# Optimization experiments

Measured on AMD Instinct MI355X. Metric: run time of the kernel, lower is better.

The kernel has to match this reference:

```python
import jax, jax.numpy as jnp
import numpy as np


def setup_inputs() -> dict:
    key = jax.random.key(0)
    k = jax.random.split(key, 5)
    C, Cb = 128, 64
    x = jax.random.normal(k[0], (8, C, 64, 64), dtype=jnp.float32)
    s_in = 1.0 / np.sqrt(C)
    s_b = 1.0 / np.sqrt(Cb)
    w_theta = jax.random.normal(k[1], (Cb, C), dtype=jnp.float32) * s_in
    w_phi = jax.random.normal(k[2], (Cb, C), dtype=jnp.float32) * s_in
    w_g = jax.random.normal(k[3], (Cb, C), dtype=jnp.float32) * s_in
    w_last = jax.random.normal(k[4], (C, Cb), dtype=jnp.float32) * s_b
    return {"x": x, "w_theta": w_theta, "w_phi": w_phi, "w_g": w_g, "w_last": w_last}


def reference(x, w_theta, w_phi, w_g, w_last):
    B, C, H, W = x.shape
    xf = x.reshape(B, C, H * W)            # [B, C, N]
    theta = jnp.einsum('kc,bcn->bkn', w_theta, xf)   # [B, Cb, N]
    phi = jnp.einsum('kc,bcn->bkn', w_phi, xf)       # [B, Cb, N]
    g = jnp.einsum('kc,bcn->bkn', w_g, xf)           # [B, Cb, N]
    # attention over spatial positions: [B, N, N]
    attn = jax.nn.softmax(jnp.einsum('bkn,bkm->bnm', theta, phi), axis=-1)
    y = jnp.einsum('bnm,bkm->bkn', attn, g)          # [B, Cb, N]
    out = jnp.einsum('ck,bkn->bcn', w_last, y).reshape(B, C, H, W)
    return out + x
```

## Files before the change

### kernel.cpp

```cpp
#include <hip/hip_runtime.h>
#include <stdint.h>

typedef _Float16 h8v __attribute__((ext_vector_type(8)));
typedef _Float16 h4v __attribute__((ext_vector_type(4)));
typedef float f4v __attribute__((ext_vector_type(4)));
typedef _Float16 f16;

#define NB 8
#define CC 128
#define CB 64
#define NN 4096
#define L2E 1.4426950408889634f

__global__ __launch_bounds__(256) void pack_w(
    const float* __restrict__ wth, const float* __restrict__ wph,
    const float* __restrict__ wg,  const float* __restrict__ wl,
    f16* __restrict__ wthp, f16* __restrict__ wphp,
    f16* __restrict__ wgp,  f16* __restrict__ wlp)
{
    const int t = blockIdx.x * 256 + threadIdx.x;
    for (int i = t; i < 8192; i += 2048){
        const int j = i & 7, lane = (i >> 3) & 63, kc = (i >> 9) & 3, ks = i >> 11;
        const int row = ks * 16 + (lane & 15);
        const int col = kc * 32 + ((lane >> 4) & 3) * 8 + j;
        wthp[i] = (f16)(wth[row * CC + col] * L2E);
        wphp[i] = (f16)(wph[row * CC + col]);
        wgp [i] = (f16)(wg [row * CC + col]);
    }
    for (int i = t; i < 8192; i += 2048){
        const int j = i & 7, lane = (i >> 3) & 63, kc = (i >> 9) & 1, cs = i >> 10;
        const int row = cs * 16 + (lane & 15);
        const int col = kc * 32 + ((lane >> 4) & 3) * 8 + j;
        wlp[i] = (f16)(wl[row * CB + col]);
    }
}

__global__ __launch_bounds__(256) void proj_kernel(
    const float* __restrict__ x, const f16* __restrict__ wthp,
    const f16* __restrict__ wphp, const f16* __restrict__ wgp,
    f16* __restrict__ thetaT, f16* __restrict__ phiT, f16* __restrict__ gbuf)
{
    __shared__ __align__(16) f16 xT[64][136];
    __shared__ __align__(16) f16 rep[4][16 * 72];
    const int b  = blockIdx.x & 7;
    const int n0 = (blockIdx.x >> 3) << 6;
    const int t  = threadIdx.x;

    #pragma unroll
    for (int i = 0; i < 8; i++){
        int v  = t + 256 * i;
        int c  = v >> 4;
        int j0 = (v & 15) << 2;
        const f4v xv = *(const f4v*)&x[((size_t)(b * CC + c)) * NN + n0 + j0];
        #pragma unroll
        for (int jj = 0; jj < 4; jj++) xT[j0 + jj][c] = (f16)xv[jj];
    }
    __syncthreads();

    const int w = t >> 6, lane = t & 63, quad = lane >> 4, l15 = lane & 15;
    const int rrow = lane >> 3, rcol = (lane & 7) * 8;

    h8v bx[4];
    #pragma unroll
    for (int kc = 0; kc < 4; kc++)
        bx[kc] = *(const h8v*)&xT[w * 16 + l15][kc * 32 + quad * 8];

    #pragma unroll
    for (int m3 = 0; m3 < 2; m3++){
        const f16* WP = (m3 == 0) ? wthp : wphp;
        f16* OUT      = (m3 == 0) ? thetaT : phiT;
        for (int ks = 0; ks < 4; ks++){
            f4v acc = {0.f, 0.f, 0.f, 0.f};
            #pragma unroll
            for (int kc = 0; kc < 4; kc++){
                const h8v af = *(const h8v*)&WP[(ks * 4 + kc) * 512 + lane * 8];
                acc = __builtin_amdgcn_mfma_f32_16x16x32_f16(af, bx[kc], acc, 0, 0, 0);
            }
            h4v pv;
            #pragma unroll
            for (int r = 0; r < 4; r++) pv[r] = (f16)acc[r];
            *(h4v*)&rep[w][l15 * 72 + ks * 16 + quad * 4] = pv;
        }
        #pragma unroll
        for (int j = 0; j < 2; j++){
            const h8v vv = *(const h8v*)&rep[w][(rrow + 8 * j) * 72 + rcol];
            *(h8v*)&OUT[((size_t)(b * NN + n0 + w * 16 + rrow + 8 * j)) * CB + rcol] = vv;
        }
    }

    h8v bw[4];
    #pragma unroll
    for (int kc = 0; kc < 4; kc++)
        bw[kc] = *(const h8v*)&wgp[(w * 4 + kc) * 512 + lane * 8];
    for (int ns = 0; ns < 4; ns++){
        f4v acc = {0.f, 0.f, 0.f, 0.f};
        #pragma unroll
        for (int kc = 0; kc < 4; kc++){
            const h8v af = *(const h8v*)&xT[ns * 16 + l15][kc * 32 + quad * 8];
            acc = __builtin_amdgcn_mfma_f32_16x16x32_f16(af, bw[kc], acc, 0, 0, 0);
        }
        h4v pv;
        #pragma unroll
        for (int r = 0; r < 4; r++) pv[r] = (f16)acc[r];
        *(h4v*)&rep[w][l15 * 72 + ns * 16 + quad * 4] = pv;
    }
    #pragma unroll
    for (int j = 0; j < 2; j++){
        const h8v vv = *(const h8v*)&rep[w][(rrow + 8 * j) * 72 + rcol];
        *(h8v*)&gbuf[((size_t)(b * CB + w * 16 + rrow + 8 * j)) * NN + n0 + rcol] = vv;
    }
}

union StageOrOut {
    struct { f16 ph[2][64 * 72]; f16 g[2][64 * 72]; } s;
    float fO[128][68];
};

__global__ __launch_bounds__(256) void attn_kernel(
    const f16* __restrict__ thetaT, const f16* __restrict__ phiT,
    const f16* __restrict__ gbuf, const f16* __restrict__ wlp,
    const float* __restrict__ x, float* __restrict__ out)
{
    __shared__ __align__(16) StageOrOut sh;
    __shared__ __align__(16) f16 plds[4][16 * 72];

    const int b  = blockIdx.x & 7;
    const int q0 = (blockIdx.x >> 3) << 6;
    const int t  = threadIdx.x;
    const int w = t >> 6, lane = t & 63, quad = lane >> 4, l15 = lane & 15;
    const int n0 = q0 + w * 16;

    const size_t trow = ((size_t)(b * NN + n0 + l15)) * CB;
    const h8v a0 = *(const h8v*)&thetaT[trow + quad * 8];
    const h8v a1 = *(const h8v*)&thetaT[trow + 32 + quad * 8];

    const int r0 = t >> 3, r1 = r0 + 32, c = (t & 7) * 8;
    const f16* pphi0 = phiT + ((size_t)(b * NN + r0)) * CB + c;
    const f16* pphi1 = phiT + ((size_t)(b * NN + r1)) * CB + c;
    const f16* pg0   = gbuf + ((size_t)(b * CB + r0)) * NN + c;
    const f16* pg1   = gbuf + ((size_t)(b * CB + r1)) * NN + c;
    const int lA = r0 * 72 + c, lB = r1 * 72 + c;

    h8v nA = *(const h8v*)pphi0;
    h8v nB = *(const h8v*)pphi1;
    h8v nC = *(const h8v*)pg0;
    h8v nD = *(const h8v*)pg1;
    *(h8v*)&sh.s.ph[0][lA] = nA;  *(h8v*)&sh.s.ph[0][lB] = nB;
    *(h8v*)&sh.s.g [0][lA] = nC;  *(h8v*)&sh.s.g [0][lB] = nD;

    float mrun = -1e30f, lrun = 0.f;
    f4v o[4];
    const f4v zf = {0.f, 0.f, 0.f, 0.f};
    #pragma unroll
    for (int tt = 0; tt < 4; tt++) o[tt] = zf;

    f16* const pw = &plds[w][0];

    for (int kb = 0; kb < 64; kb++){
        const int pb = kb & 1;
        __syncthreads();
        if (kb < 63){
            pphi0 += (size_t)64 * CB;  pphi1 += (size_t)64 * CB;
            pg0 += 64;                 pg1 += 64;
            nA = *(const h8v*)pphi0;   nB = *(const h8v*)pphi1;
            nC = *(const h8v*)pg0;     nD = *(const h8v*)pg1;
        }

        f4v s[4];
        #pragma unroll
        for (int tt = 0; tt < 4; tt++){
            const f16* pr = &sh.s.ph[pb][(tt * 16 + l15) * 72];
            const h8v pb0 = *(const h8v*)(pr + quad * 8);
            const h8v pb1 = *(const h8v*)(pr + 32 + quad * 8);
            f4v sv = zf;
            sv = __builtin_amdgcn_mfma_f32_16x16x32_f16(pb0, a0, sv, 0, 0, 0);
            sv = __builtin_amdgcn_mfma_f32_16x16x32_f16(pb1, a1, sv, 0, 0, 0);
            s[tt] = sv;
        }
        float smax = fmaxf(fmaxf(s[0][0], s[0][1]), fmaxf(s[0][2], s[0][3]));
        #pragma unroll
        for (int tt = 1; tt < 4; tt++)
            smax = fmaxf(smax, fmaxf(fmaxf(s[tt][0], s[tt][1]), fmaxf(s[tt][2], s[tt][3])));
        smax = fmaxf(smax, __shfl_xor(smax, 16));
        smax = fmaxf(smax, __shfl_xor(smax, 32));
        const float mn = fmaxf(mrun, smax);
        const float alpha = __builtin_amdgcn_exp2f(mrun - mn);
        mrun = mn;
        float lsum = 0.f;
        #pragma unroll
        for (int tt = 0; tt < 4; tt++){
            h4v pv;
            #pragma unroll
            for (int r = 0; r < 4; r++){
                float p = __builtin_amdgcn_exp2f(s[tt][r] - mn);
                lsum += p;
                pv[r] = (f16)p;
            }
            *(h4v*)&pw[l15 * 72 + tt * 16 + quad * 4] = pv;
        }
        lrun = lrun * alpha + lsum;
        #pragma unroll
        for (int tt = 0; tt < 4; tt++)
            #pragma unroll
            for (int r = 0; r < 4; r++)
                o[tt][r] *= alpha;

        const h8v pa0 = *(const h8v*)&pw[l15 * 72 + quad * 8];
        const h8v pa1 = *(const h8v*)&pw[l15 * 72 + 32 + quad * 8];

        #pragma unroll
        for (int tt = 0; tt < 4; tt++){
            const f16* gr = &sh.s.g[pb][(tt * 16 + l15) * 72];
            const h8v gb0 = *(const h8v*)(gr + quad * 8);
            const h8v gb1 = *(const h8v*)(gr + 32 + quad * 8);
            o[tt] = __builtin_amdgcn_mfma_f32_16x16x32_f16(gb0, pa0, o[tt], 0, 0, 0);
            o[tt] = __builtin_amdgcn_mfma_f32_16x16x32_f16(gb1, pa1, o[tt], 0, 0, 0);
        }

        if (kb < 63){
            const int nb = pb ^ 1;
            *(h8v*)&sh.s.ph[nb][lA] = nA;  *(h8v*)&sh.s.ph[nb][lB] = nB;
            *(h8v*)&sh.s.g [nb][lA] = nC;  *(h8v*)&sh.s.g [nb][lB] = nD;
        }
    }

    lrun += __shfl_xor(lrun, 16);
    lrun += __shfl_xor(lrun, 32);
    const float inv = 1.0f / lrun;

    #pragma unroll
    for (int tt = 0; tt < 4; tt++){
        h4v yv;
        #pragma unroll
        for (int r = 0; r < 4; r++) yv[r] = (f16)(o[tt][r] * inv);
        *(h4v*)&pw[l15 * 72 + tt * 16 + quad * 4] = yv;
    }

    __syncthreads();

    const h8v yB0 = *(const h8v*)&pw[l15 * 72 + quad * 8];
    const h8v yB1 = *(const h8v*)&pw[l15 * 72 + 32 + quad * 8];
    #pragma unroll
    for (int cs = 0; cs < 8; cs++){
        const h8v wa0 = *(const h8v*)&wlp[(cs * 2 + 0) * 512 + lane * 8];
        const h8v wa1 = *(const h8v*)&wlp[(cs * 2 + 1) * 512 + lane * 8];
        f4v acc = zf;
        acc = __builtin_amdgcn_mfma_f32_16x16x32_f16(wa0, yB0, acc, 0, 0, 0);
        acc = __builtin_amdgcn_mfma_f32_16x16x32_f16(wa1, yB1, acc, 0, 0, 0);
        #pragma unroll
        for (int r = 0; r < 4; r++)
            sh.fO[cs * 16 + quad * 4 + r][w * 16 + l15] = acc[r];
    }
    __syncthreads();

    #pragma unroll
    for (int i = 0; i < 8; i++){
        const int row = i * 16 + (t >> 4);
        const int nf  = (t & 15) * 4;
        const f4v v = *(const f4v*)&sh.fO[row][nf];
        const size_t idx = ((size_t)(b * CC + row)) * NN + q0 + nf;
        const f4v xv = *(const f4v*)&x[idx];
        f4v ov;
        #pragma unroll
        for (int r = 0; r < 4; r++) ov[r] = v[r] + xv[r];
        *(f4v*)&out[idx] = ov;
    }
}

extern "C" void kernel_launch(void* const* d_in, const int* in_sizes, int n_in,
                              void* d_out, int out_size, void* d_ws, size_t ws_size,
                              hipStream_t stream)
{
    const float* x   = (const float*)d_in[0];
    const float* wth = (const float*)d_in[1];
    const float* wph = (const float*)d_in[2];
    const float* wg  = (const float*)d_in[3];
    const float* wl  = (const float*)d_in[4];
    float* out = (float*)d_out;

    f16* thetaT = (f16*)d_ws;
    f16* phiT   = thetaT + (size_t)NB * NN * CB;
    f16* gbuf   = phiT   + (size_t)NB * NN * CB;
    f16* wthp   = gbuf   + (size_t)NB * NN * CB;
    f16* wphp   = wthp + 8192;
    f16* wgp    = wphp + 8192;
    f16* wlp    = wgp  + 8192;

    pack_w<<<8, 256, 0, stream>>>(wth, wph, wg, wl, wthp, wphp, wgp, wlp);
    proj_kernel<<<NB * 64, 256, 0, stream>>>(x, wthp, wphp, wgp, thetaT, phiT, gbuf);
    attn_kernel<<<NB * 64, 256, 0, stream>>>(thetaT, phiT, gbuf, wlp, x, out);
}
```

Baseline: 160.4 us.

## Process 32 query rows per wave and rescale softmax lazily

Each wave now computes two 16-row query tiles against every staged phi/g tile in LDS. That doubles MFMA work per LDS load and halves the grid to 256 blocks with launch_bounds(256,1). The online softmax skips rescaling the running max and accumulators unless some lane's max grows by more than 8 in the exp2 domain. The output projection and residual epilogue run in two halves that reuse the shared fO buffer. The risks are higher register pressure and fewer resident waves per CU, which can hurt latency hiding, and the lazy rescale allows unnormalized probabilities up to 256 in fp16.

```diff
diff --git a/kernel.cpp b/kernel.cpp
--- a/kernel.cpp
+++ b/kernel.cpp
@@ -116,23 +116,26 @@
     float fO[128][68];
 };
 
-__global__ __launch_bounds__(256) void attn_kernel(
+__global__ __launch_bounds__(256, 1) void attn_kernel(
     const f16* __restrict__ thetaT, const f16* __restrict__ phiT,
     const f16* __restrict__ gbuf, const f16* __restrict__ wlp,
     const float* __restrict__ x, float* __restrict__ out)
 {
     __shared__ __align__(16) StageOrOut sh;
-    __shared__ __align__(16) f16 plds[4][16 * 72];
+    __shared__ __align__(16) f16 plds[4][32 * 72];
 
     const int b  = blockIdx.x & 7;
-    const int q0 = (blockIdx.x >> 3) << 6;
+    const int q0 = (blockIdx.x >> 3) << 7;
     const int t  = threadIdx.x;
     const int w = t >> 6, lane = t & 63, quad = lane >> 4, l15 = lane & 15;
-    const int n0 = q0 + w * 16;
-
-    const size_t trow = ((size_t)(b * NN + n0 + l15)) * CB;
-    const h8v a0 = *(const h8v*)&thetaT[trow + quad * 8];
-    const h8v a1 = *(const h8v*)&thetaT[trow + 32 + quad * 8];
+    const int n0 = q0 + w * 32;
+
+    const size_t trow0 = ((size_t)(b * NN + n0 + l15)) * CB;
+    const size_t trow1 = ((size_t)(b * NN + n0 + 16 + l15)) * CB;
+    const h8v a0 = *(const h8v*)&thetaT[trow0 + quad * 8];
+    const h8v a1 = *(const h8v*)&thetaT[trow0 + 32 + quad * 8];
+    const h8v a2 = *(const h8v*)&thetaT[trow1 + quad * 8];
+    const h8v a3 = *(const h8v*)&thetaT[trow1 + 32 + quad * 8];
 
     const int r0 = t >> 3, r1 = r0 + 32, c = (t & 7) * 8;
     const f16* pphi0 = phiT + ((size_t)(b * NN + r0)) * CB + c;
@@ -148,11 +151,11 @@
     *(h8v*)&sh.s.ph[0][lA] = nA;  *(h8v*)&sh.s.ph[0][lB] = nB;
     *(h8v*)&sh.s.g [0][lA] = nC;  *(h8v*)&sh.s.g [0][lB] = nD;
 
-    float mrun = -1e30f, lrun = 0.f;
-    f4v o[4];
+    float mrun0 = -1e30f, mrun1 = -1e30f, lrun0 = 0.f, lrun1 = 0.f;
     const f4v zf = {0.f, 0.f, 0.f, 0.f};
-    #pragma unroll
-    for (int tt = 0; tt < 4; tt++) o[tt] = zf;
+    f4v o[4][2];
+    #pragma unroll
+    for (int tt = 0; tt < 4; tt++){ o[tt][0] = zf; o[tt][1] = zf; }
 
     f16* const pw = &plds[w][0];
 
@@ -166,7 +169,7 @@
             nC = *(const h8v*)pg0;     nD = *(const h8v*)pg1;
         }
 
-        f4v s[4];
+        f4v s0[4], s1[4];
         #pragma unroll
         for (int tt = 0; tt < 4; tt++){
             const f16* pr = &sh.s.ph[pb][(tt * 16 + l15) * 72];
@@ -175,46 +178,72 @@
             f4v sv = zf;
             sv = __builtin_amdgcn_mfma_f32_16x16x32_f16(pb0, a0, sv, 0, 0, 0);
             sv = __builtin_amdgcn_mfma_f32_16x16x32_f16(pb1, a1, sv, 0, 0, 0);
-            s[tt] = sv;
-        }
-        float smax = fmaxf(fmaxf(s[0][0], s[0][1]), fmaxf(s[0][2], s[0][3]));
-        #pragma unroll
-        for (int tt = 1; tt < 4; tt++)
-            smax = fmaxf(smax, fmaxf(fmaxf(s[tt][0], s[tt][1]), fmaxf(s[tt][2], s[tt][3])));
-        smax = fmaxf(smax, __shfl_xor(smax, 16));
-        smax = fmaxf(smax, __shfl_xor(smax, 32));
-        const float mn = fmaxf(mrun, smax);
-        const float alpha = __builtin_amdgcn_exp2f(mrun - mn);
-        mrun = mn;
-        float lsum = 0.f;
+            s0[tt] = sv;
+            f4v sw = zf;
+            sw = __builtin_amdgcn_mfma_f32_16x16x32_f16(pb0, a2, sw, 0, 0, 0);
+            sw = __builtin_amdgcn_mfma_f32_16x16x32_f16(pb1, a3, sw, 0, 0, 0);
+            s1[tt] = sw;
+        }
+
+        float smax0 = fmaxf(fmaxf(s0[0][0], s0[0][1]), fmaxf(s0[0][2], s0[0][3]));
+        float smax1 = fmaxf(fmaxf(s1[0][0], s1[0][1]), fmaxf(s1[0][2], s1[0][3]));
+        #pragma unroll
+        for (int tt = 1; tt < 4; tt++){
+            smax0 = fmaxf(smax0, fmaxf(fmaxf(s0[tt][0], s0[tt][1]), fmaxf(s0[tt][2], s0[tt][3])));
+            smax1 = fmaxf(smax1, fmaxf(fmaxf(s1[tt][0], s1[tt][1]), fmaxf(s1[tt][2], s1[tt][3])));
+        }
+        smax0 = fmaxf(smax0, __shfl_xor(smax0, 16));
+        smax0 = fmaxf(smax0, __shfl_xor(smax0, 32));
+        smax1 = fmaxf(smax1, __shfl_xor(smax1, 16));
+        smax1 = fmaxf(smax1, __shfl_xor(smax1, 32));
+
+        const float d = fmaxf(smax0 - mrun0, smax1 - mrun1);
+        if (__any(d > 8.f)){
+            const float mn0 = fmaxf(mrun0, smax0);
+            const float mn1 = fmaxf(mrun1, smax1);
+            const float al0 = __builtin_amdgcn_exp2f(mrun0 - mn0);
+            const float al1 = __builtin_amdgcn_exp2f(mrun1 - mn1);
+            mrun0 = mn0; mrun1 = mn1;
+            lrun0 *= al0; lrun1 *= al1;
+            #pragma unroll
+            for (int tt = 0; tt < 4; tt++)
+                #pragma unroll
+                for (int r = 0; r < 4; r++){
+                    o[tt][0][r] *= al0;
+                    o[tt][1][r] *= al1;
+                }
+        }
+
+        float ls0 = 0.f, ls1 = 0.f;
         #pragma unroll
         for (int tt = 0; tt < 4; tt++){
-            h4v pv;
+            h4v pv0, pv1;
             #pragma unroll
             for (int r = 0; r < 4; r++){
-                float p = __builtin_amdgcn_exp2f(s[tt][r] - mn);
-                lsum += p;
-                pv[r] = (f16)p;
+                float p = __builtin_amdgcn_exp2f(s0[tt][r] - mrun0);
+                ls0 += p;  pv0[r] = (f16)p;
+                float q = __builtin_amdgcn_exp2f(s1[tt][r] - mrun1);
+                ls1 += q;  pv1[r] = (f16)q;
             }
-            *(h4v*)&pw[l15 * 72 + tt * 16 + quad * 4] = pv;
-        }
-        lrun = lrun * alpha + lsum;
-        #pragma unroll
-        for (int tt = 0; tt < 4; tt++)
-            #pragma unroll
-            for (int r = 0; r < 4; r++)
-                o[tt][r] *= alpha;
-
-        const h8v pa0 = *(const h8v*)&pw[l15 * 72 + quad * 8];
-        const h8v pa1 = *(const h8v*)&pw[l15 * 72 + 32 + quad * 8];
+            *(h4v*)&pw[l15 * 72 + tt * 16 + quad * 4]        = pv0;
+            *(h4v*)&pw[(16 + l15) * 72 + tt * 16 + quad * 4] = pv1;
+        }
+        lrun0 += ls0;  lrun1 += ls1;
+
+        const h8v paA = *(const h8v*)&pw[l15 * 72 + quad * 8];
+        const h8v paB = *(const h8v*)&pw[l15 * 72 + 32 + quad * 8];
+        const h8v paC = *(const h8v*)&pw[(16 + l15) * 72 + quad * 8];
+        const h8v paD = *(const h8v*)&pw[(16 + l15) * 72 + 32 + quad * 8];
 
         #pragma unroll
         for (int tt = 0; tt < 4; tt++){
             const f16* gr = &sh.s.g[pb][(tt * 16 + l15) * 72];
             const h8v gb0 = *(const h8v*)(gr + quad * 8);
             const h8v gb1 = *(const h8v*)(gr + 32 + quad * 8);
-            o[tt] = __builtin_amdgcn_mfma_f32_16x16x32_f16(gb0, pa0, o[tt], 0, 0, 0);
-            o[tt] = __builtin_amdgcn_mfma_f32_16x16x32_f16(gb1, pa1, o[tt], 0, 0, 0);
+            o[tt][0] = __builtin_amdgcn_mfma_f32_16x16x32_f16(gb0, paA, o[tt][0], 0, 0, 0);
+            o[tt][0] = __builtin_amdgcn_mfma_f32_16x16x32_f16(gb1, paB, o[tt][0], 0, 0, 0);
+            o[tt][1] = __builtin_amdgcn_mfma_f32_16x16x32_f16(gb0, paC, o[tt][1], 0, 0, 0);
+            o[tt][1] = __builtin_amdgcn_mfma_f32_16x16x32_f16(gb1, paD, o[tt][1], 0, 0, 0);
         }
 
         if (kb < 63){
@@ -224,41 +253,90 @@
         }
     }
 
-    lrun += __shfl_xor(lrun, 16);
-    lrun += __shfl_xor(lrun, 32);
-    const float inv = 1.0f / lrun;
+    lrun0 += __shfl_xor(lrun0, 16);
+    lrun0 += __shfl_xor(lrun0, 32);
+    lrun1 += __shfl_xor(lrun1, 16);
+    lrun1 += __shfl_xor(lrun1, 32);
+    const float inv0 = 1.0f / lrun0;
+    const float inv1 = 1.0f / lrun1;
 
     #pragma unroll
     for (int tt = 0; tt < 4; tt++){
-        h4v yv;
-        #pragma unroll
-        for (int r = 0; r < 4; r++) yv[r] = (f16)(o[tt][r] * inv);
-        *(h4v*)&pw[l15 * 72 + tt * 16 + quad * 4] = yv;
-    }
-
-    __syncthreads();
+        h4v y0, y1;
+        #pragma unroll
+        for (int r = 0; r < 4; r++){
+            y0[r] = (f16)(o[tt][0][r] * inv0);
+            y1[r] = (f16)(o[tt][1][r] * inv1);
+        }
+        *(h4v*)&pw[l15 * 72 + tt * 16 + quad * 4]        = y0;
+        *(h4v*)&pw[(16 + l15) * 72 + tt * 16 + quad * 4] = y1;
+    }
 
     const h8v yB0 = *(const h8v*)&pw[l15 * 72 + quad * 8];
     const h8v yB1 = *(const h8v*)&pw[l15 * 72 + 32 + quad * 8];
-    #pragma unroll
-    for (int cs = 0; cs < 8; cs++){
-        const h8v wa0 = *(const h8v*)&wlp[(cs * 2 + 0) * 512 + lane * 8];
-        const h8v wa1 = *(const h8v*)&wlp[(cs * 2 + 1) * 512 + lane * 8];
-        f4v acc = zf;
-        acc = __builtin_amdgcn_mfma_f32_16x16x32_f16(wa0, yB0, acc, 0, 0, 0);
-        acc = __builtin_amdgcn_mfma_f32_16x16x32_f16(wa1, yB1, acc, 0, 0, 0);
-        #pragma unroll
-        for (int r = 0; r < 4; r++)
-            sh.fO[cs * 16 + quad * 4 + r][w * 16 + l15] = acc[r];
-    }
-    __syncthreads();
-
+    const h8v yB2 = *(const h8v*)&pw[(16 + l15) * 72 + quad * 8];
+    const h8v yB3 = *(const h8v*)&pw[(16 + l15) * 72 + 32 + quad * 8];
+
+    __syncthreads();
+
+    if (w < 2){
+        #pragma unroll
+        for (int cs = 0; cs < 8; cs++){
+            const h8v wa0 = *(const h8v*)&wlp[(cs * 2 + 0) * 512 + lane * 8];
+            const h8v wa1 = *(const h8v*)&wlp[(cs * 2 + 1) * 512 + lane * 8];
+            f4v acc = zf;
+            acc = __builtin_amdgcn_mfma_f32_16x16x32_f16(wa0, yB0, acc, 0, 0, 0);
+            acc = __builtin_amdgcn_mfma_f32_16x16x32_f16(wa1, yB1, acc, 0, 0, 0);
+            f4v acc1 = zf;
+            acc1 = __builtin_amdgcn_mfma_f32_16x16x32_f16(wa0, yB2, acc1, 0, 0, 0);
+            acc1 = __builtin_amdgcn_mfma_f32_16x16x32_f16(wa1, yB3, acc1, 0, 0, 0);
+            #pragma unroll
+            for (int r = 0; r < 4; r++){
+                sh.fO[cs * 16 + quad * 4 + r][w * 32 + l15]      = acc[r];
+                sh.fO[cs * 16 + quad * 4 + r][w * 32 + 16 + l15] = acc1[r];
+            }
+        }
+    }
+    __syncthreads();
     #pragma unroll
     for (int i = 0; i < 8; i++){
         const int row = i * 16 + (t >> 4);
         const int nf  = (t & 15) * 4;
         const f4v v = *(const f4v*)&sh.fO[row][nf];
         const size_t idx = ((size_t)(b * CC + row)) * NN + q0 + nf;
+        const f4v xv = *(const f4v*)&x[idx];
+        f4v ov;
+        #pragma unroll
+        for (int r = 0; r < 4; r++) ov[r] = v[r] + xv[r];
+        *(f4v*)&out[idx] = ov;
+    }
+    __syncthreads();
+
+    if (w >= 2){
+        #pragma unroll
+        for (int cs = 0; cs < 8; cs++){
+            const h8v wa0 = *(const h8v*)&wlp[(cs * 2 + 0) * 512 + lane * 8];
+            const h8v wa1 = *(const h8v*)&wlp[(cs * 2 + 1) * 512 + lane * 8];
+            f4v acc = zf;
+            acc = __builtin_amdgcn_mfma_f32_16x16x32_f16(wa0, yB0, acc, 0, 0, 0);
+            acc = __builtin_amdgcn_mfma_f32_16x16x32_f16(wa1, yB1, acc, 0, 0, 0);
+            f4v acc1 = zf;
+            acc1 = __builtin_amdgcn_mfma_f32_16x16x32_f16(wa0, yB2, acc1, 0, 0, 0);
+            acc1 = __builtin_amdgcn_mfma_f32_16x16x32_f16(wa1, yB3, acc1, 0, 0, 0);
+            #pragma unroll
+            for (int r = 0; r < 4; r++){
+                sh.fO[cs * 16 + quad * 4 + r][(w - 2) * 32 + l15]      = acc[r];
+                sh.fO[cs * 16 + quad * 4 + r][(w - 2) * 32 + 16 + l15] = acc1[r];
+            }
+        }
+    }
+    __syncthreads();
+    #pragma unroll
+    for (int i = 0; i < 8; i++){
+        const int row = i * 16 + (t >> 4);
+        const int nf  = (t & 15) * 4;
+        const f4v v = *(const f4v*)&sh.fO[row][nf];
+        const size_t idx = ((size_t)(b * CC + row)) * NN + q0 + 64 + nf;
         const f4v xv = *(const f4v*)&x[idx];
         f4v ov;
         #pragma unroll
@@ -288,5 +366,5 @@
 
     pack_w<<<8, 256, 0, stream>>>(wth, wph, wg, wl, wthp, wphp, wgp, wlp);
     proj_kernel<<<NB * 64, 256, 0, stream>>>(x, wthp, wphp, wgp, thetaT, phiT, gbuf);
-    attn_kernel<<<NB * 64, 256, 0, stream>>>(thetaT, phiT, gbuf, wlp, x, out);
+    attn_kernel<<<NB * 32, 256, 0, stream>>>(thetaT, phiT, gbuf, wlp, x, out);
 }
```

Result: slower. 170.8 us (+6.5%).

## Load phi and g fragments directly from global, drop LDS staging and syncs

Applied to the files above, without the earlier changes.

The attention loop no longer stages phi and g tiles through double-buffered shared memory with a block barrier per iteration; each wave loads its MFMA operand fragments straight from global memory, relying on L2 and cache reuse across waves. The online-softmax rescale is skipped unless the running max grows by more than a threshold (lazy rescaling). Launch bounds request two blocks per CU. This removes 64 barriers and the LDS round trip but duplicates global loads across the four waves and exposes load latency without explicit prefetch.

```diff
diff --git a/kernel.cpp b/kernel.cpp
--- a/kernel.cpp
+++ b/kernel.cpp
@@ -111,17 +111,12 @@
     }
 }
 
-union StageOrOut {
-    struct { f16 ph[2][64 * 72]; f16 g[2][64 * 72]; } s;
-    float fO[128][68];
-};
-
-__global__ __launch_bounds__(256) void attn_kernel(
+__global__ __launch_bounds__(256, 2) void attn_kernel(
     const f16* __restrict__ thetaT, const f16* __restrict__ phiT,
     const f16* __restrict__ gbuf, const f16* __restrict__ wlp,
     const float* __restrict__ x, float* __restrict__ out)
 {
-    __shared__ __align__(16) StageOrOut sh;
+    __shared__ __align__(16) float fO[128][68];
     __shared__ __align__(16) f16 plds[4][16 * 72];
 
     const int b  = blockIdx.x & 7;
@@ -134,93 +129,79 @@
     const h8v a0 = *(const h8v*)&thetaT[trow + quad * 8];
     const h8v a1 = *(const h8v*)&thetaT[trow + 32 + quad * 8];
 
-    const int r0 = t >> 3, r1 = r0 + 32, c = (t & 7) * 8;
-    const f16* pphi0 = phiT + ((size_t)(b * NN + r0)) * CB + c;
-    const f16* pphi1 = phiT + ((size_t)(b * NN + r1)) * CB + c;
-    const f16* pg0   = gbuf + ((size_t)(b * CB + r0)) * NN + c;
-    const f16* pg1   = gbuf + ((size_t)(b * CB + r1)) * NN + c;
-    const int lA = r0 * 72 + c, lB = r1 * 72 + c;
-
-    h8v nA = *(const h8v*)pphi0;
-    h8v nB = *(const h8v*)pphi1;
-    h8v nC = *(const h8v*)pg0;
-    h8v nD = *(const h8v*)pg1;
-    *(h8v*)&sh.s.ph[0][lA] = nA;  *(h8v*)&sh.s.ph[0][lB] = nB;
-    *(h8v*)&sh.s.g [0][lA] = nC;  *(h8v*)&sh.s.g [0][lB] = nD;
+    const f16* const pph = phiT + ((size_t)(b * NN + l15)) * CB + quad * 8;
+    const f16* const pgg = gbuf + ((size_t)(b * CB + l15)) * NN + quad * 8;
 
     float mrun = -1e30f, lrun = 0.f;
+    const f4v zf = {0.f, 0.f, 0.f, 0.f};
     f4v o[4];
-    const f4v zf = {0.f, 0.f, 0.f, 0.f};
     #pragma unroll
     for (int tt = 0; tt < 4; tt++) o[tt] = zf;
 
     f16* const pw = &plds[w][0];
 
     for (int kb = 0; kb < 64; kb++){
-        const int pb = kb & 1;
-        __syncthreads();
-        if (kb < 63){
-            pphi0 += (size_t)64 * CB;  pphi1 += (size_t)64 * CB;
-            pg0 += 64;                 pg1 += 64;
-            nA = *(const h8v*)pphi0;   nB = *(const h8v*)pphi1;
-            nC = *(const h8v*)pg0;     nD = *(const h8v*)pg1;
+        const f16* pp = pph + (size_t)(kb * 64) * CB;
+        const f16* pg = pgg + kb * 64;
+
+        h8v f0[4], f1[4], g0[4], g1[4];
+        #pragma unroll
+        for (int tt = 0; tt < 4; tt++){
+            f0[tt] = *(const h8v*)(pp + (size_t)(tt * 16) * CB);
+            f1[tt] = *(const h8v*)(pp + (size_t)(tt * 16) * CB + 32);
+            g0[tt] = *(const h8v*)(pg + (size_t)(tt * 16) * NN);
+            g1[tt] = *(const h8v*)(pg + (size_t)(tt * 16) * NN + 32);
         }
 
         f4v s[4];
         #pragma unroll
         for (int tt = 0; tt < 4; tt++){
-            const f16* pr = &sh.s.ph[pb][(tt * 16 + l15) * 72];
-            const h8v pb0 = *(const h8v*)(pr + quad * 8);
-            const h8v pb1 = *(const h8v*)(pr + 32 + quad * 8);
             f4v sv = zf;
-            sv = __builtin_amdgcn_mfma_f32_16x16x32_f16(pb0, a0, sv, 0, 0, 0);
-            sv = __builtin_amdgcn_mfma_f32_16x16x32_f16(pb1, a1, sv, 0, 0, 0);
+            sv = __builtin_amdgcn_mfma_f32_16x16x32_f16(f0[tt], a0, sv, 0, 0, 0);
+            sv = __builtin_amdgcn_mfma_f32_16x16x32_f16(f1[tt], a1, sv, 0, 0, 0);
             s[tt] = sv;
         }
+
         float smax = fmaxf(fmaxf(s[0][0], s[0][1]), fmaxf(s[0][2], s[0][3]));
         #pragma unroll
         for (int tt = 1; tt < 4; tt++)
             smax = fmaxf(smax, fmaxf(fmaxf(s[tt][0], s[tt][1]), fmaxf(s[tt][2], s[tt][3])));
         smax = fmaxf(smax, __shfl_xor(smax, 16));
         smax = fmaxf(smax, __shfl_xor(smax, 32));
-        const float mn = fmaxf(mrun, smax);
-        const float alpha = __builtin_amdgcn_exp2f(mrun - mn);
-        mrun = mn;
+
+        if (__any(smax - mrun > 8.f)){
+            const float mn = fmaxf(mrun, smax);
+            const float alpha = __builtin_amdgcn_exp2f(mrun - mn);
+            mrun = mn;
+            lrun *= alpha;
+            #pragma unroll
+            for (int tt = 0; tt < 4; tt++)
+                #pragma unroll
+                for (int r = 0; r < 4; r++)
+                    o[tt][r] *= alpha;
+        }
+
         float lsum = 0.f;
         #pragma unroll
         for (int tt = 0; tt < 4; tt++){
             h4v pv;
             #pragma unroll
             for (int r = 0; r < 4; r++){
-                float p = __builtin_amdgcn_exp2f(s[tt][r] - mn);
+                float p = __builtin_amdgcn_exp2f(s[tt][r] - mrun);
                 lsum += p;
                 pv[r] = (f16)p;
             }
             *(h4v*)&pw[l15 * 72 + tt * 16 + quad * 4] = pv;
         }
-        lrun = lrun * alpha + lsum;
-        #pragma unroll
-        for (int tt = 0; tt < 4; tt++)
-            #pragma unroll
-            for (int r = 0; r < 4; r++)
-                o[tt][r] *= alpha;
+        lrun += lsum;
 
         const h8v pa0 = *(const h8v*)&pw[l15 * 72 + quad * 8];
         const h8v pa1 = *(const h8v*)&pw[l15 * 72 + 32 + quad * 8];
 
         #pragma unroll
         for (int tt = 0; tt < 4; tt++){
-            const f16* gr = &sh.s.g[pb][(tt * 16 + l15) * 72];
-            const h8v gb0 = *(const h8v*)(gr + quad * 8);
-            const h8v gb1 = *(const h8v*)(gr + 32 + quad * 8);
-            o[tt] = __builtin_amdgcn_mfma_f32_16x16x32_f16(gb0, pa0, o[tt], 0, 0, 0);
-            o[tt] = __builtin_amdgcn_mfma_f32_16x16x32_f16(gb1, pa1, o[tt], 0, 0, 0);
-        }
-
-        if (kb < 63){
-            const int nb = pb ^ 1;
-            *(h8v*)&sh.s.ph[nb][lA] = nA;  *(h8v*)&sh.s.ph[nb][lB] = nB;
-            *(h8v*)&sh.s.g [nb][lA] = nC;  *(h8v*)&sh.s.g [nb][lB] = nD;
+            o[tt] = __builtin_amdgcn_mfma_f32_16x16x32_f16(g0[tt], pa0, o[tt], 0, 0, 0);
+            o[tt] = __builtin_amdgcn_mfma_f32_16x16x32_f16(g1[tt], pa1, o[tt], 0, 0, 0);
         }
     }
 
@@ -235,8 +216,6 @@
         for (int r = 0; r < 4; r++) yv[r] = (f16)(o[tt][r] * inv);
         *(h4v*)&pw[l15 * 72 + tt * 16 + quad * 4] = yv;
     }
-
-    __syncthreads();
 
     const h8v yB0 = *(const h8v*)&pw[l15 * 72 + quad * 8];
     const h8v yB1 = *(const h8v*)&pw[l15 * 72 + 32 + quad * 8];
@@ -249,7 +228,7 @@
         acc = __builtin_amdgcn_mfma_f32_16x16x32_f16(wa1, yB1, acc, 0, 0, 0);
         #pragma unroll
         for (int r = 0; r < 4; r++)
-            sh.fO[cs * 16 + quad * 4 + r][w * 16 + l15] = acc[r];
+            fO[cs * 16 + quad * 4 + r][w * 16 + l15] = acc[r];
     }
     __syncthreads();
 
@@ -257,7 +236,7 @@
     for (int i = 0; i < 8; i++){
         const int row = i * 16 + (t >> 4);
         const int nf  = (t & 15) * 4;
-        const f4v v = *(const f4v*)&sh.fO[row][nf];
+        const f4v v = *(const f4v*)&fO[row][nf];
         const size_t idx = ((size_t)(b * CC + row)) * NN + q0 + nf;
         const f4v xv = *(const f4v*)&x[idx];
         f4v ov;
```

Result: slower. 310.8 us (+93.8%).
